# Kernel optimization log

Hardware: AMD Instinct MI355X
Metric: run time of the kernel (lower is better)

Reference implementation:

```python
import jax, jax.numpy as jnp
import numpy as np

PE_DIM = 40  # pe_dim; gaussian PE scale factor = pe_dim // 2


def _batched_linear(x, wb):
    # x: [B, N, D], wb: [B, D+1, H] (last row is bias)
    return jnp.einsum('bnd,bdh->bnh', x, wb[:, :-1, :]) + wb[:, -1:, :]


def setup_inputs() -> dict:
    key = jax.random.key(0)
    ks = jax.random.split(key, 8)
    B, N = 16, 16384
    H = 256
    pe_out = 3 * PE_DIM  # 120
    s = 0.05  # keep ReLU-chain activations bounded
    return {
        'x': jax.random.normal(ks[0], (B, N, 3), dtype=jnp.float32),
        'wb0': jax.random.normal(ks[1], (B, pe_out + 1, H), dtype=jnp.float32) * s,
        'wb1': jax.random.normal(ks[2], (B, H + 1, H), dtype=jnp.float32) * s,
        'wb2': jax.random.normal(ks[3], (B, H + 1, H), dtype=jnp.float32) * s,
        'wb3': jax.random.normal(ks[4], (B, H + 1, H), dtype=jnp.float32) * s,
        'wb4': jax.random.normal(ks[5], (B, H + 1, H), dtype=jnp.float32) * s,
        'wb_out': jax.random.normal(ks[6], (B, H + 1, 1), dtype=jnp.float32) * s,
        'rand_freqs': jax.random.normal(ks[7], (3 * (PE_DIM // 2), 3), dtype=jnp.float32),  # feat_sigma=1
    }


def reference(x, wb0, wb1, wb2, wb3, wb4, wb_out, rand_freqs):
    # Gaussian positional encoding: k = x . (rand_freqs * pe_dim//2)
    k = jnp.einsum('bnd,fd->bnf', x, rand_freqs * (PE_DIM // 2))  # [B,N,60]
    h = jnp.concatenate([jnp.sin(k), jnp.cos(k)], axis=-1)        # [B,N,120]
    for wb in (wb0, wb1, wb2, wb3, wb4):
        h = jax.nn.relu(_batched_linear(h, wb))
    out = _batched_linear(h, wb_out)  # [B,N,1]
    return out
```

## Files before the change

### kernel.cpp

```cpp
#include <hip/hip_runtime.h>
#include <hip/hip_bf16.h>


#define H 256
#define MT 64
#define PE_NF 60

typedef __attribute__((ext_vector_type(8))) short s16x8;
typedef __attribute__((ext_vector_type(4))) float f32x4;

#define BATCH_BYTES (size_t)589824
#define BATCH_ELEMS (size_t)294912

static __device__ __forceinline__ unsigned short f2bf(float v) {
  unsigned int u = __float_as_uint(v);
  return (unsigned short)((u + 0x7FFFu + ((u >> 16) & 1u)) >> 16);
}
static __device__ __forceinline__ int hswz(int row, int chunk) {
  return (chunk & ~7) | ((chunk ^ row) & 7);
}

static __device__ __forceinline__ void bar_raw() {
  asm volatile("s_barrier" ::: "memory");
}
static __device__ __forceinline__ void bar_lgkm() {
  asm volatile("s_waitcnt lgkmcnt(0)\n\ts_barrier" ::: "memory");
}

__global__ __launch_bounds__(256) void prep_weights(
    const float* __restrict__ wb0, const float* __restrict__ wb1,
    const float* __restrict__ wb2, const float* __restrict__ wb3,
    const float* __restrict__ wb4,
    unsigned short* __restrict__ wpk, float* __restrict__ biases) {
  int z = blockIdx.z;
  int li = z >> 4, b = z & 15;
  int k0 = blockIdx.x * 32;
  int n0 = blockIdx.y * 32;
  int Ks;
  const float* src;
  unsigned short* dst;
  if (li == 0) {
    Ks = 120;
    if (k0 >= 128) return;
    src = wb0 + (size_t)b * 121 * H;
    dst = wpk + b * BATCH_ELEMS;
  } else {
    Ks = 256;
    const float* srcs[4] = {wb1, wb2, wb3, wb4};
    src = srcs[li - 1] + (size_t)b * 257 * H;
    dst = wpk + b * BATCH_ELEMS + 32768 + (size_t)(li - 1) * 65536;
  }
  __shared__ float tile[32][33];
  int t = threadIdx.x;
  int tx = t & 31, ty = t >> 5;
#pragma unroll
  for (int i = 0; i < 4; ++i) {
    int k = k0 + ty + i * 8;
    tile[ty + i * 8][tx] = (k < Ks) ? src[(size_t)k * H + n0 + tx] : 0.f;
  }
  if (k0 == 0 && ty == 0)
    biases[((size_t)li * 16 + b) * H + n0 + tx] = src[(size_t)Ks * H + n0 + tx];
  __syncthreads();
  if (t < 128) {
    int nn = t & 31, kg = t >> 5;
    int n = n0 + nn;
    int kt = k0 >> 5;
    union { unsigned short us[8]; s16x8 v; } pk;
#pragma unroll
    for (int j = 0; j < 8; ++j) pk.us[j] = f2bf(tile[kg * 8 + j][nn]);
    *(s16x8*)&dst[(size_t)(kt * 16 + (n >> 4)) * 512 + (kg * 16 + (n & 15)) * 8] = pk.v;
  }
}

template <int NKT, bool LAST>
static __device__ __forceinline__ void mlp_layer(
    const char*& fp, const float* __restrict__ bl,
    unsigned short* __restrict__ h_s, const float* __restrict__ wout_s,
    const int rlane, const int kgrp, const int wc, const int l,
    s16x8 (&wf)[4], float* psum) {
  static_assert((NKT & 1) == 0, "parity needs even NKT");
  f32x4 acc[4][4];
#pragma unroll
  for (int ct = 0; ct < 4; ++ct) {
    f32x4 bini = *(const f32x4*)(bl + wc * 64 + ct * 16 + kgrp * 4);
#pragma unroll
    for (int rt = 0; rt < 4; ++rt) acc[rt][ct] = bini;
  }

  const char* hb = (const char*)h_s;
  const unsigned be = rlane * 512 + hswz(rlane, kgrp) * 16;
  const unsigned bo = rlane * 512 + hswz(rlane, 4 + kgrp) * 16;

  unsigned koff = 0;
#pragma unroll 2
  for (int kt = 0; kt < NKT; ++kt) {
    s16x8 af[4];
    const unsigned base = ((kt & 1) ? bo : be) + koff;
#pragma unroll
    for (int rt = 0; rt < 4; ++rt)
      af[rt] = *(const s16x8*)(hb + base + rt * 8192);
    if (kt & 1) koff += 128;

    __builtin_amdgcn_s_setprio(1);
#pragma unroll
    for (int rt = 0; rt < 4; ++rt)
#pragma unroll
      for (int ct = 0; ct < 4; ++ct)
        acc[rt][ct] = __builtin_amdgcn_mfma_f32_16x16x32_bf16(
            wf[ct], af[rt], acc[rt][ct], 0, 0, 0);
    __builtin_amdgcn_s_setprio(0);

#pragma unroll
    for (int c = 0; c < 4; ++c)
      wf[c] = *(const s16x8*)(fp + c * 1024);
    fp += 16384;
  }

  if constexpr (LAST) {
    float p[4];
#pragma unroll
    for (int rt = 0; rt < 4; ++rt) {
      float s = 0.f;
#pragma unroll
      for (int ct = 0; ct < 4; ++ct) {
        f32x4 wv = *(const f32x4*)(wout_s + wc * 64 + ct * 16 + kgrp * 4);
#pragma unroll
        for (int g = 0; g < 4; ++g)
          s += fmaxf(acc[rt][ct][g], 0.f) * wv[g];
      }
      s += __shfl_xor(s, 16);
      s += __shfl_xor(s, 32);
      p[rt] = s;
    }
    if (l < 16) {
#pragma unroll
      for (int rt = 0; rt < 4; ++rt)
        psum[wc * 64 + rt * 16 + l] = p[rt];
    }
  } else {
    bar_raw();
    const int sub = (kgrp & 1) * 4;
    const int cbase = wc * 8 + (kgrp >> 1);
#pragma unroll
    for (int rt = 0; rt < 4; ++rt) {
      const int m = rt * 16 + rlane;
      const int rowb = m * 256;
#pragma unroll
      for (int ct = 0; ct < 4; ++ct) {
        const int cs = hswz(m, cbase + ct * 2);
        float v0 = fmaxf(acc[rt][ct][0], 0.f);
        float v1 = fmaxf(acc[rt][ct][1], 0.f);
        float v2 = fmaxf(acc[rt][ct][2], 0.f);
        float v3 = fmaxf(acc[rt][ct][3], 0.f);
        union { __hip_bfloat162 h2[2]; uint2 u; } pk;
        pk.h2[0] = __float22bfloat162_rn(float2{v0, v1});
        pk.h2[1] = __float22bfloat162_rn(float2{v2, v3});
        *(uint2*)&h_s[rowb + cs * 8 + sub] = pk.u;
      }
    }
    bar_lgkm();
  }
}

__global__ __launch_bounds__(256, 4) void hyponerf_main(
    const float* __restrict__ x, const float* __restrict__ rfreq,
    const float* __restrict__ wbout, const unsigned short* __restrict__ wpk,
    const float* __restrict__ biases, float* __restrict__ out) {
  __shared__ __align__(16) unsigned short h_s[MT * 256];
  __shared__ float fr_s[PE_NF * 3];
  __shared__ float x_s[MT * 3];
  __shared__ float wout_s[H + 1];
  __shared__ float psum[4 * 64];

  int bid = blockIdx.x;
  int logical = (bid & 7) * 512 + (bid >> 3);
  int b  = logical >> 8;
  int mt = logical & 255;

  int t = threadIdx.x;
  int wc = t >> 6, l = t & 63;
  int rlane = l & 15;
  int kgrp  = l >> 4;

  const char* fp = (const char*)wpk + b * BATCH_BYTES
                 + (size_t)wc * 4096 + (size_t)l * 16;

  s16x8 wf[4];
#pragma unroll
  for (int c = 0; c < 4; ++c) wf[c] = *(const s16x8*)(fp + c * 1024);
  fp += 16384;

  const float* xg = x + ((size_t)b * 16384 + (size_t)mt * MT) * 3;
  for (int i = t; i < MT * 3; i += 256) x_s[i] = xg[i];
  for (int i = t; i < PE_NF * 3; i += 256) fr_s[i] = rfreq[i] * 20.0f;
  for (int i = t; i < H + 1; i += 256) wout_s[i] = wbout[(size_t)b * (H + 1) + i];
  bar_lgkm();

  {
    int r = t >> 2;
    int q = t & 3;
    float x0 = x_s[r * 3 + 0], x1 = x_s[r * 3 + 1], x2 = x_s[r * 3 + 2];
    int rowb = r * 256;
#pragma unroll
    for (int cc = 0; cc < 4; ++cc) {
      int ch = q * 4 + cc;
      union { unsigned short us[8]; s16x8 v; } pk;
#pragma unroll
      for (int j = 0; j < 8; ++j) {
        int n = ch * 8 + j;
        float v = 0.f;
        if (n < 60) {
          float kv = x0 * fr_s[n * 3] + x1 * fr_s[n * 3 + 1] + x2 * fr_s[n * 3 + 2];
          v = __sinf(kv);
        } else if (n < 120) {
          int f = n - 60;
          float kv = x0 * fr_s[f * 3] + x1 * fr_s[f * 3 + 1] + x2 * fr_s[f * 3 + 2];
          v = __cosf(kv);
        }
        pk.us[j] = f2bf(v);
      }
      *(s16x8*)&h_s[rowb + hswz(r, ch) * 8] = pk.v;
    }
  }
  bar_lgkm();

  const float* bb = biases + (size_t)b * H;
  mlp_layer<4, false>(fp, bb + 0 * 16 * H, h_s, wout_s, rlane, kgrp, wc, l,
                      wf, psum);
  mlp_layer<8, false>(fp, bb + 1 * 16 * H, h_s, wout_s, rlane, kgrp, wc, l,
                      wf, psum);
  mlp_layer<8, false>(fp, bb + 2 * 16 * H, h_s, wout_s, rlane, kgrp, wc, l,
                      wf, psum);
  mlp_layer<8, false>(fp, bb + 3 * 16 * H, h_s, wout_s, rlane, kgrp, wc, l,
                      wf, psum);
  mlp_layer<8, true >(fp, bb + 4 * 16 * H, h_s, wout_s, rlane, kgrp, wc, l,
                      wf, psum);

  bar_lgkm();
  if (t < MT) {
    float s = psum[t] + psum[64 + t] + psum[128 + t] + psum[192 + t];
    out[(size_t)b * 16384 + (size_t)mt * MT + t] = s + wout_s[H];
  }
}

extern "C" void kernel_launch(void* const* d_in, const int* in_sizes, int n_in,
                              void* d_out, int out_size, void* d_ws, size_t ws_size,
                              hipStream_t stream) {
  const float* x     = (const float*)d_in[0];
  const float* wb0   = (const float*)d_in[1];
  const float* wb1   = (const float*)d_in[2];
  const float* wb2   = (const float*)d_in[3];
  const float* wb3   = (const float*)d_in[4];
  const float* wb4   = (const float*)d_in[5];
  const float* wbout = (const float*)d_in[6];
  const float* rfreq = (const float*)d_in[7];
  float* out = (float*)d_out;

  char* ws = (char*)d_ws;
  unsigned short* wpk = (unsigned short*)ws;
  float* biases = (float*)(ws + 16 * BATCH_BYTES);

  prep_weights<<<dim3(8, 8, 80), 256, 0, stream>>>(wb0, wb1, wb2, wb3, wb4,
                                                   wpk, biases);
  hyponerf_main<<<dim3(4096), 256, 0, stream>>>(x, rfreq, wbout, wpk,
                                                biases, out);
}
```

Before: 168.3 us.

## Rotate K-tile order per wave to defer inter-layer barrier

Each wave now starts a layer's K loop at its own pair of K-tiles (wc*2), which are exactly the h_s columns it wrote itself in the previous layer's epilogue. The trailing barrier after the epilogue is removed, and one barrier is placed after the first two K-tiles instead. This lets waves begin MFMA work without waiting for all others. The weight-prefetch addressing becomes explicit per-layer pointers with a per-wave rotation offset, which adds address arithmetic. The correctness of the shared-memory read/write overlap depends on this ownership mapping.

```diff
diff --git a/kernel.cpp b/kernel.cpp
--- a/kernel.cpp
+++ b/kernel.cpp
@@ -72,13 +72,36 @@
   }
 }
 
-template <int NKT, bool LAST>
+#define KT_BODY(KTP, RELOAD_PTR, DO_RELOAD)                                   \
+  {                                                                           \
+    const int ktp_ = (KTP);                                                   \
+    s16x8 af[4];                                                              \
+    const unsigned base_ = ((ktp_ & 1) ? bo : be) + (ktp_ >> 1) * 128;        \
+    _Pragma("unroll")                                                         \
+    for (int rt = 0; rt < 4; ++rt)                                            \
+      af[rt] = *(const s16x8*)(hb + base_ + rt * 8192);                       \
+    __builtin_amdgcn_s_setprio(1);                                            \
+    _Pragma("unroll")                                                         \
+    for (int rt = 0; rt < 4; ++rt)                                            \
+      _Pragma("unroll")                                                       \
+      for (int ct = 0; ct < 4; ++ct)                                          \
+        acc[rt][ct] = __builtin_amdgcn_mfma_f32_16x16x32_bf16(                \
+            wf[ct], af[rt], acc[rt][ct], 0, 0, 0);                            \
+    __builtin_amdgcn_s_setprio(0);                                            \
+    if (DO_RELOAD) {                                                          \
+      const char* nb_ = (RELOAD_PTR);                                         \
+      _Pragma("unroll")                                                       \
+      for (int c = 0; c < 4; ++c)                                             \
+        wf[c] = *(const s16x8*)(nb_ + c * 1024);                              \
+    }                                                                         \
+  }
+
+template <int NKT, bool FIRST, bool LAST>
 static __device__ __forceinline__ void mlp_layer(
-    const char*& fp, const float* __restrict__ bl,
+    const char* fpl, const char* fpn, const float* __restrict__ bl,
     unsigned short* __restrict__ h_s, const float* __restrict__ wout_s,
     const int rlane, const int kgrp, const int wc, const int l,
     s16x8 (&wf)[4], float* psum) {
-  static_assert((NKT & 1) == 0, "parity needs even NKT");
   f32x4 acc[4][4];
 #pragma unroll
   for (int ct = 0; ct < 4; ++ct) {
@@ -88,32 +111,29 @@
   }
 
   const char* hb = (const char*)h_s;
-  const unsigned be = rlane * 512 + hswz(rlane, kgrp) * 16;
-  const unsigned bo = rlane * 512 + hswz(rlane, 4 + kgrp) * 16;
-
-  unsigned koff = 0;
+  const unsigned be = rlane * 512 + ((kgrp ^ (rlane & 7)) & 7) * 16;
+  const unsigned bo = rlane * 512 + (((4 + kgrp) ^ (rlane & 7)) & 7) * 16;
+
+  if constexpr (FIRST) {
 #pragma unroll 2
-  for (int kt = 0; kt < NKT; ++kt) {
-    s16x8 af[4];
-    const unsigned base = ((kt & 1) ? bo : be) + koff;
-#pragma unroll
-    for (int rt = 0; rt < 4; ++rt)
-      af[rt] = *(const s16x8*)(hb + base + rt * 8192);
-    if (kt & 1) koff += 128;
-
-    __builtin_amdgcn_s_setprio(1);
-#pragma unroll
-    for (int rt = 0; rt < 4; ++rt)
-#pragma unroll
-      for (int ct = 0; ct < 4; ++ct)
-        acc[rt][ct] = __builtin_amdgcn_mfma_f32_16x16x32_bf16(
-            wf[ct], af[rt], acc[rt][ct], 0, 0, 0);
-    __builtin_amdgcn_s_setprio(0);
-
-#pragma unroll
-    for (int c = 0; c < 4; ++c)
-      wf[c] = *(const s16x8*)(fp + c * 1024);
-    fp += 16384;
+    for (int i = 0; i < NKT; ++i) {
+      KT_BODY(i,
+              (i + 1 < NKT) ? (fpl + (i + 1) * 16384) : fpn,
+              (i + 1 < NKT) || !LAST)
+    }
+  } else {
+#pragma unroll
+    for (int i = 0; i < 2; ++i) {
+      KT_BODY(wc * 2 + i, fpl + ((wc * 2 + i + 1) & (NKT - 1)) * 16384, true)
+    }
+    bar_lgkm();
+#pragma unroll 2
+    for (int i = 2; i < NKT; ++i) {
+      KT_BODY((wc * 2 + i) & (NKT - 1),
+              (i + 1 < NKT) ? (fpl + ((wc * 2 + i + 1) & (NKT - 1)) * 16384)
+                            : fpn,
+              (i + 1 < NKT) || !LAST)
+    }
   }
 
   if constexpr (LAST) {
@@ -158,7 +178,6 @@
         *(uint2*)&h_s[rowb + cs * 8 + sub] = pk.u;
       }
     }
-    bar_lgkm();
   }
 }
 
@@ -182,13 +201,18 @@
   int rlane = l & 15;
   int kgrp  = l >> 4;
 
-  const char* fp = (const char*)wpk + b * BATCH_BYTES
-                 + (size_t)wc * 4096 + (size_t)l * 16;
+  const char* base = (const char*)wpk + b * BATCH_BYTES
+                   + (size_t)wc * 4096 + (size_t)l * 16;
+  const char* L0 = base;
+  const char* L1 = base + 65536;
+  const char* L2 = base + 196608;
+  const char* L3 = base + 327680;
+  const char* L4 = base + 458752;
+  const unsigned rot = (unsigned)wc * 32768;
 
   s16x8 wf[4];
 #pragma unroll
-  for (int c = 0; c < 4; ++c) wf[c] = *(const s16x8*)(fp + c * 1024);
-  fp += 16384;
+  for (int c = 0; c < 4; ++c) wf[c] = *(const s16x8*)(L0 + c * 1024);
 
   const float* xg = x + ((size_t)b * 16384 + (size_t)mt * MT) * 3;
   for (int i = t; i < MT * 3; i += 256) x_s[i] = xg[i];
@@ -225,16 +249,16 @@
   bar_lgkm();
 
   const float* bb = biases + (size_t)b * H;
-  mlp_layer<4, false>(fp, bb + 0 * 16 * H, h_s, wout_s, rlane, kgrp, wc, l,
-                      wf, psum);
-  mlp_layer<8, false>(fp, bb + 1 * 16 * H, h_s, wout_s, rlane, kgrp, wc, l,
-                      wf, psum);
-  mlp_layer<8, false>(fp, bb + 2 * 16 * H, h_s, wout_s, rlane, kgrp, wc, l,
-                      wf, psum);
-  mlp_layer<8, false>(fp, bb + 3 * 16 * H, h_s, wout_s, rlane, kgrp, wc, l,
-                      wf, psum);
-  mlp_layer<8, true >(fp, bb + 4 * 16 * H, h_s, wout_s, rlane, kgrp, wc, l,
-                      wf, psum);
+  mlp_layer<4, true,  false>(L0, L1 + rot, bb + 0 * 16 * H, h_s, wout_s,
+                             rlane, kgrp, wc, l, wf, psum);
+  mlp_layer<8, false, false>(L1, L2 + rot, bb + 1 * 16 * H, h_s, wout_s,
+                             rlane, kgrp, wc, l, wf, psum);
+  mlp_layer<8, false, false>(L2, L3 + rot, bb + 2 * 16 * H, h_s, wout_s,
+                             rlane, kgrp, wc, l, wf, psum);
+  mlp_layer<8, false, false>(L3, L4 + rot, bb + 3 * 16 * H, h_s, wout_s,
+                             rlane, kgrp, wc, l, wf, psum);
+  mlp_layer<8, false, true >(L4, L4, bb + 4 * 16 * H, h_s, wout_s,
+                             rlane, kgrp, wc, l, wf, psum);
 
   bar_lgkm();
   if (t < MT) {
```

Result: slower. 197.7 us (+17.5%).

## Split row tile into two halves and overlap epilogue with other half's MMA

Applied to the files above, without the earlier changes.

The 64-row activation tile is split into two 32-row halves with separate accumulators. Each layer's k-loop now runs per half, and the ReLU/bf16 writeback of one half is interleaved with the MFMA loop of the other. A weight-pointer handoff between the two passes keeps the register prefetch going. This aims to hide the epilogue and barrier cost behind matrix work, but each weight fragment is now loaded twice per layer and each k-step issues half as many MFMAs per weight load.

```diff
diff --git a/kernel.cpp b/kernel.cpp
--- a/kernel.cpp
+++ b/kernel.cpp
@@ -20,9 +20,6 @@
   return (chunk & ~7) | ((chunk ^ row) & 7);
 }
 
-static __device__ __forceinline__ void bar_raw() {
-  asm volatile("s_barrier" ::: "memory");
-}
 static __device__ __forceinline__ void bar_lgkm() {
   asm volatile("s_waitcnt lgkmcnt(0)\n\ts_barrier" ::: "memory");
 }
@@ -72,93 +69,101 @@
   }
 }
 
-template <int NKT, bool LAST>
-static __device__ __forceinline__ void mlp_layer(
-    const char*& fp, const float* __restrict__ bl,
-    unsigned short* __restrict__ h_s, const float* __restrict__ wout_s,
-    const int rlane, const int kgrp, const int wc, const int l,
-    s16x8 (&wf)[4], float* psum) {
-  static_assert((NKT & 1) == 0, "parity needs even NKT");
-  f32x4 acc[4][4];
+template <int NKT>
+static __device__ __forceinline__ void kloop_seg(
+    const char*& fp, const char*& fpo, const float* __restrict__ bl,
+    const char* hb, const unsigned be, const unsigned bo,
+    const int wc, const int kgrp, s16x8 (&wf)[4], f32x4 (&acc)[2][4]) {
 #pragma unroll
   for (int ct = 0; ct < 4; ++ct) {
     f32x4 bini = *(const f32x4*)(bl + wc * 64 + ct * 16 + kgrp * 4);
-#pragma unroll
-    for (int rt = 0; rt < 4; ++rt) acc[rt][ct] = bini;
-  }
-
-  const char* hb = (const char*)h_s;
-  const unsigned be = rlane * 512 + hswz(rlane, kgrp) * 16;
-  const unsigned bo = rlane * 512 + hswz(rlane, 4 + kgrp) * 16;
-
-  unsigned koff = 0;
+    acc[0][ct] = bini;
+    acc[1][ct] = bini;
+  }
 #pragma unroll 2
-  for (int kt = 0; kt < NKT; ++kt) {
-    s16x8 af[4];
-    const unsigned base = ((kt & 1) ? bo : be) + koff;
-#pragma unroll
-    for (int rt = 0; rt < 4; ++rt)
-      af[rt] = *(const s16x8*)(hb + base + rt * 8192);
-    if (kt & 1) koff += 128;
-
+  for (int kt = 0; kt < NKT - 1; ++kt) {
+    s16x8 af[2];
+    const unsigned base = ((kt & 1) ? bo : be) + (kt >> 1) * 128;
+    af[0] = *(const s16x8*)(hb + base);
+    af[1] = *(const s16x8*)(hb + base + 8192);
     __builtin_amdgcn_s_setprio(1);
 #pragma unroll
-    for (int rt = 0; rt < 4; ++rt)
+    for (int rt = 0; rt < 2; ++rt)
 #pragma unroll
       for (int ct = 0; ct < 4; ++ct)
         acc[rt][ct] = __builtin_amdgcn_mfma_f32_16x16x32_bf16(
             wf[ct], af[rt], acc[rt][ct], 0, 0, 0);
     __builtin_amdgcn_s_setprio(0);
-
 #pragma unroll
     for (int c = 0; c < 4; ++c)
       wf[c] = *(const s16x8*)(fp + c * 1024);
     fp += 16384;
   }
-
-  if constexpr (LAST) {
-    float p[4];
-#pragma unroll
-    for (int rt = 0; rt < 4; ++rt) {
-      float s = 0.f;
-#pragma unroll
-      for (int ct = 0; ct < 4; ++ct) {
-        f32x4 wv = *(const f32x4*)(wout_s + wc * 64 + ct * 16 + kgrp * 4);
-#pragma unroll
-        for (int g = 0; g < 4; ++g)
-          s += fmaxf(acc[rt][ct][g], 0.f) * wv[g];
-      }
-      s += __shfl_xor(s, 16);
-      s += __shfl_xor(s, 32);
-      p[rt] = s;
+  {
+    s16x8 af[2];
+    const unsigned base = (((NKT - 1) & 1) ? bo : be) + ((NKT - 1) >> 1) * 128;
+    af[0] = *(const s16x8*)(hb + base);
+    af[1] = *(const s16x8*)(hb + base + 8192);
+    __builtin_amdgcn_s_setprio(1);
+#pragma unroll
+    for (int rt = 0; rt < 2; ++rt)
+#pragma unroll
+      for (int ct = 0; ct < 4; ++ct)
+        acc[rt][ct] = __builtin_amdgcn_mfma_f32_16x16x32_bf16(
+            wf[ct], af[rt], acc[rt][ct], 0, 0, 0);
+    __builtin_amdgcn_s_setprio(0);
+#pragma unroll
+    for (int c = 0; c < 4; ++c)
+      wf[c] = *(const s16x8*)(fpo + c * 1024);
+    fpo += 16384;
+  }
+}
+
+static __device__ __forceinline__ void epi_half(
+    f32x4 (&acc)[2][4], char* hb, const int rlane, const int kgrp,
+    const int wc) {
+  const int sub = (kgrp & 1) * 4;
+  const int cbase = wc * 8 + (kgrp >> 1);
+#pragma unroll
+  for (int rt = 0; rt < 2; ++rt) {
+    const int m = rt * 16 + rlane;
+    const int rowb = m * 512;
+#pragma unroll
+    for (int ct = 0; ct < 4; ++ct) {
+      const int cs = hswz(m, cbase + ct * 2);
+      float v0 = fmaxf(acc[rt][ct][0], 0.f);
+      float v1 = fmaxf(acc[rt][ct][1], 0.f);
+      float v2 = fmaxf(acc[rt][ct][2], 0.f);
+      float v3 = fmaxf(acc[rt][ct][3], 0.f);
+      union { __hip_bfloat162 h2[2]; uint2 u; } pk;
+      pk.h2[0] = __float22bfloat162_rn(float2{v0, v1});
+      pk.h2[1] = __float22bfloat162_rn(float2{v2, v3});
+      *(uint2*)(hb + rowb + cs * 16 + sub * 2) = pk.u;
     }
-    if (l < 16) {
-#pragma unroll
-      for (int rt = 0; rt < 4; ++rt)
-        psum[wc * 64 + rt * 16 + l] = p[rt];
+  }
+}
+
+static __device__ __forceinline__ void proj_half(
+    f32x4 (&acc)[2][4], const float* __restrict__ wout_s, float* psum,
+    const int l, const int wc, const int kgrp, const int half) {
+  float p[2];
+#pragma unroll
+  for (int rt = 0; rt < 2; ++rt) {
+    float s = 0.f;
+#pragma unroll
+    for (int ct = 0; ct < 4; ++ct) {
+      f32x4 wv = *(const f32x4*)(wout_s + wc * 64 + ct * 16 + kgrp * 4);
+#pragma unroll
+      for (int g = 0; g < 4; ++g)
+        s += fmaxf(acc[rt][ct][g], 0.f) * wv[g];
     }
-  } else {
-    bar_raw();
-    const int sub = (kgrp & 1) * 4;
-    const int cbase = wc * 8 + (kgrp >> 1);
-#pragma unroll
-    for (int rt = 0; rt < 4; ++rt) {
-      const int m = rt * 16 + rlane;
-      const int rowb = m * 256;
-#pragma unroll
-      for (int ct = 0; ct < 4; ++ct) {
-        const int cs = hswz(m, cbase + ct * 2);
-        float v0 = fmaxf(acc[rt][ct][0], 0.f);
-        float v1 = fmaxf(acc[rt][ct][1], 0.f);
-        float v2 = fmaxf(acc[rt][ct][2], 0.f);
-        float v3 = fmaxf(acc[rt][ct][3], 0.f);
-        union { __hip_bfloat162 h2[2]; uint2 u; } pk;
-        pk.h2[0] = __float22bfloat162_rn(float2{v0, v1});
-        pk.h2[1] = __float22bfloat162_rn(float2{v2, v3});
-        *(uint2*)&h_s[rowb + cs * 8 + sub] = pk.u;
-      }
-    }
-    bar_lgkm();
+    s += __shfl_xor(s, 16);
+    s += __shfl_xor(s, 32);
+    p[rt] = s;
+  }
+  if (l < 16) {
+    psum[wc * 64 + half * 32 + l]      = p[0];
+    psum[wc * 64 + half * 32 + 16 + l] = p[1];
   }
 }
 
@@ -182,13 +187,19 @@
   int rlane = l & 15;
   int kgrp  = l >> 4;
 
-  const char* fp = (const char*)wpk + b * BATCH_BYTES
-                 + (size_t)wc * 4096 + (size_t)l * 16;
+  char* hA = (char*)h_s;
+  char* hB = (char*)h_s + 16384;
+  const unsigned be = rlane * 512 + ((kgrp ^ (rlane & 7)) & 7) * 16;
+  const unsigned bo = rlane * 512 + (((4 + kgrp) ^ (rlane & 7)) & 7) * 16;
+
+  const char* fpA = (const char*)wpk + b * BATCH_BYTES
+                  + (size_t)wc * 4096 + (size_t)l * 16;
+  const char* fpB = fpA;
 
   s16x8 wf[4];
 #pragma unroll
-  for (int c = 0; c < 4; ++c) wf[c] = *(const s16x8*)(fp + c * 1024);
-  fp += 16384;
+  for (int c = 0; c < 4; ++c) wf[c] = *(const s16x8*)(fpA + c * 1024);
+  fpA += 16384;
 
   const float* xg = x + ((size_t)b * 16384 + (size_t)mt * MT) * 3;
   for (int i = t; i < MT * 3; i += 256) x_s[i] = xg[i];
@@ -200,7 +211,8 @@
     int r = t >> 2;
     int q = t & 3;
     float x0 = x_s[r * 3 + 0], x1 = x_s[r * 3 + 1], x2 = x_s[r * 3 + 2];
-    int rowb = r * 256;
+    char* hb = (r < 32) ? hA : hB;
+    int rowb = (r & 31) * 512;
 #pragma unroll
     for (int cc = 0; cc < 4; ++cc) {
       int ch = q * 4 + cc;
@@ -219,24 +231,42 @@
         }
         pk.us[j] = f2bf(v);
       }
-      *(s16x8*)&h_s[rowb + hswz(r, ch) * 8] = pk.v;
+      *(s16x8*)(hb + rowb + hswz(r & 31, ch) * 16) = pk.v;
     }
   }
   bar_lgkm();
 
   const float* bb = biases + (size_t)b * H;
-  mlp_layer<4, false>(fp, bb + 0 * 16 * H, h_s, wout_s, rlane, kgrp, wc, l,
-                      wf, psum);
-  mlp_layer<8, false>(fp, bb + 1 * 16 * H, h_s, wout_s, rlane, kgrp, wc, l,
-                      wf, psum);
-  mlp_layer<8, false>(fp, bb + 2 * 16 * H, h_s, wout_s, rlane, kgrp, wc, l,
-                      wf, psum);
-  mlp_layer<8, false>(fp, bb + 3 * 16 * H, h_s, wout_s, rlane, kgrp, wc, l,
-                      wf, psum);
-  mlp_layer<8, true >(fp, bb + 4 * 16 * H, h_s, wout_s, rlane, kgrp, wc, l,
-                      wf, psum);
-
-  bar_lgkm();
+  f32x4 accA[2][4], accB[2][4];
+
+  kloop_seg<4>(fpA, fpB, bb, hA, be, bo, wc, kgrp, wf, accA);
+  bar_lgkm();
+  kloop_seg<4>(fpB, fpA, bb, hB, be, bo, wc, kgrp, wf, accB);
+  epi_half(accA, hA, rlane, kgrp, wc);
+  bar_lgkm();
+
+#pragma unroll 1
+  for (int li = 1; li < 4; ++li) {
+    const float* bl = bb + (size_t)li * 16 * H;
+    kloop_seg<8>(fpA, fpB, bl, hA, be, bo, wc, kgrp, wf, accA);
+    epi_half(accB, hB, rlane, kgrp, wc);
+    bar_lgkm();
+    kloop_seg<8>(fpB, fpA, bl, hB, be, bo, wc, kgrp, wf, accB);
+    epi_half(accA, hA, rlane, kgrp, wc);
+    bar_lgkm();
+  }
+
+  {
+    const float* bl = bb + (size_t)4 * 16 * H;
+    kloop_seg<8>(fpA, fpB, bl, hA, be, bo, wc, kgrp, wf, accA);
+    epi_half(accB, hB, rlane, kgrp, wc);
+    bar_lgkm();
+    kloop_seg<8>(fpB, fpA, bl, hB, be, bo, wc, kgrp, wf, accB);
+    proj_half(accA, wout_s, psum, l, wc, kgrp, 0);
+    proj_half(accB, wout_s, psum, l, wc, kgrp, 1);
+    bar_lgkm();
+  }
+
   if (t < MT) {
     float s = psum[t] + psum[64 + t] + psum[128 + t] + psum[192 + t];
     out[(size_t)b * 16384 + (size_t)mt * MT + t] = s + wout_s[H];
```

Result: slower. 270.7 us (+60.8%).
